# Kernel optimization log

Hardware: AMD Instinct MI355X
Metric: run time of the kernel (lower is better)

## Reference

```python
import jax, jax.numpy as jnp
import numpy as np

NUM_HEADS = 8
SIGMA = 1.0
LAMBDA_INIT = 0.1
GAMMA_INIT = 0.001


def _pos_encoding(H, W, d_model):
    # 2D sinusoidal encoding: first half encodes x (width), second half y (height)
    d = d_model // 2
    div = jnp.exp(jnp.arange(0, d, 2, dtype=jnp.float32) * (-np.log(10000.0) / d))
    xs = jnp.arange(W, dtype=jnp.float32)[:, None] * div  # (W, d//2)
    ys = jnp.arange(H, dtype=jnp.float32)[:, None] * div  # (H, d//2)
    pe_x = jnp.stack([jnp.sin(xs), jnp.cos(xs)], axis=-1).reshape(W, d)
    pe_y = jnp.stack([jnp.sin(ys), jnp.cos(ys)], axis=-1).reshape(H, d)
    pe = jnp.concatenate([
        jnp.broadcast_to(pe_x[None, :, :], (H, W, d)),
        jnp.broadcast_to(pe_y[:, None, :], (H, W, d)),
    ], axis=-1)
    return pe  # (H, W, d_model)


def _distance_map(H, W, sigma):
    # exp(-euclidean_dist / sigma) between all flattened pixel positions
    yy, xx = jnp.meshgrid(jnp.arange(H, dtype=jnp.float32), jnp.arange(W, dtype=jnp.float32), indexing='ij')
    coords = jnp.stack([yy.reshape(-1), xx.reshape(-1)], axis=-1)  # (HW, 2)
    d2 = jnp.sum((coords[:, None, :] - coords[None, :, :]) ** 2, axis=-1)
    return jnp.exp(-jnp.sqrt(d2) / sigma)  # (HW, HW)


def _conv1x1(x, w, b):
    # 1x1 conv == channel matmul; x: (B,C,H,W), w: (O,C), b: (O,)
    return jnp.einsum('bchw,oc->bohw', x, w) + b[None, :, None, None]


def setup_inputs() -> dict:
    key = jax.random.key(0)
    ks = jax.random.split(key, 9)
    B, C, H, W = 2, 256, 48, 48
    d_model = 256
    inp = {
        'x': jax.random.normal(ks[0], (B, C, H, W), dtype=jnp.float32),
        'Wq': jax.random.normal(ks[1], (d_model, C), dtype=jnp.float32) * 0.01,
        'bq': jnp.zeros((d_model,), dtype=jnp.float32),
        'Wk': jax.random.normal(ks[2], (d_model, C), dtype=jnp.float32) * 0.01,
        'bk': jnp.zeros((d_model,), dtype=jnp.float32),
        'Wv': jax.random.normal(ks[3], (d_model, C), dtype=jnp.float32) * 0.01,
        'bv': jnp.zeros((d_model,), dtype=jnp.float32),
        'Wo': jax.random.normal(ks[4], (C, d_model), dtype=jnp.float32) * 0.01,
        'bo': jnp.zeros((C,), dtype=jnp.float32),
        'lambda_dist': jnp.float32(LAMBDA_INIT),
        'gamma': jnp.float32(GAMMA_INIT),
    }
    return inp


def reference(x, Wq, bq, Wk, bk, Wv, bv, Wo, bo, lambda_dist, gamma):
    B, C, H, W = x.shape
    d_model = Wq.shape[0]
    d_k = d_model // NUM_HEADS
    pe = _pos_encoding(H, W, d_model).transpose(2, 0, 1)[None]  # (1, d_model, H, W)
    dm = _distance_map(H, W, SIGMA)                              # (HW, HW)

    q = _conv1x1(x, Wq, bq) + pe
    k = _conv1x1(x, Wk, bk) + pe
    v = _conv1x1(x, Wv, bv)

    def heads(t):
        return t.reshape(B, NUM_HEADS, d_k, H * W).transpose(0, 1, 3, 2)  # (B,h,HW,d_k)

    Q, K, V = heads(q), heads(k), heads(v)
    scores = jnp.einsum('bhnd,bhmd->bhnm', Q, K) / jnp.sqrt(jnp.float32(d_k))
    scores = scores + (lambda_dist * dm)[None, None]  # 'exp' distance prior bias
    attn = jax.nn.softmax(scores, axis=-1)
    out = jnp.einsum('bhnm,bhmd->bhnd', attn, V)
    out = out.transpose(0, 1, 3, 2).reshape(B, d_model, H, W)
    fused = gamma * out  # simple weighted fusion, single (self) branch
    return x + _conv1x1(fused, Wo, bo)
```

## Files before the change

### kernel.cpp

```cpp
#include <hip/hip_runtime.h>

#define HW 2304
#define SW 48
#define DMODEL 256
#define NHEADS 8
#define DK 32
#define BATCH 2

typedef unsigned short u16;
typedef __attribute__((ext_vector_type(8))) short short8;
typedef __attribute__((ext_vector_type(4))) float f32x4;

__device__ __forceinline__ float bf2f(u16 v) {
  union { unsigned int u; float f; } c; c.u = ((unsigned int)v) << 16; return c.f;
}
__device__ __forceinline__ u16 f2bf(float f) {
  union { unsigned int u; float f; } c; c.f = f;
  unsigned int u = c.u;
  unsigned int r = (u + 0x7FFFu + ((u >> 16) & 1u)) >> 16;
  return (u16)r;
}
__device__ __forceinline__ int div48(int n) { return (n * 87382) >> 22; }
__device__ __forceinline__ int swz(int row, int k) {
  return ((row >> 4) << 12) + ((k >> 3) << 7) + ((row & 15) << 3) + (k & 7);
}

#define DTAB_N 9032

__global__ __launch_bounds__(256) void prep_kernel(
    const float* __restrict__ x,
    const float* __restrict__ Wq, const float* __restrict__ Wk,
    const float* __restrict__ Wv, const float* __restrict__ Wo,
    const float* __restrict__ lam_p,
    u16* __restrict__ xt, u16* __restrict__ Wb, u16* __restrict__ dtabb) {
  int bid = blockIdx.x;
  int t = threadIdx.x;
  if (bid < 288) {
    int b = bid / 144, r = bid % 144;
    int c0 = (r / 36) * 64, n0 = (r % 36) * 64;
    __shared__ u16 sh[64][72];
#pragma unroll
    for (int p = 0; p < 4; ++p) {
      int row = (t >> 4) + p * 16;
      int col4 = (t & 15) * 4;
      float4 v = *(const float4*)(x + (size_t)(b * DMODEL + c0 + row) * HW +
                                  n0 + col4);
      sh[col4 + 0][row] = f2bf(v.x);
      sh[col4 + 1][row] = f2bf(v.y);
      sh[col4 + 2][row] = f2bf(v.z);
      sh[col4 + 3][row] = f2bf(v.w);
    }
    __syncthreads();
    u16* xtb = xt + (size_t)b * HW * DMODEL;
#pragma unroll
    for (int q = 0; q < 2; ++q) {
      int nrow = t >> 2;
      int c8 = (t & 3) * 8 + q * 32;
      *(uint4*)(xtb + swz(n0 + nrow, c0 + c8)) = *(const uint4*)&sh[nrow][c8];
    }
  } else if (bid < 544) {
    int idx = (bid - 288) * 1024 + t * 4;
    int which = idx >> 16, off = idx & 65535;
    int m = off >> 8, k = off & 255;
    const float* src = (which == 0) ? Wq : (which == 1) ? Wk
                       : (which == 2) ? Wv : Wo;
    float4 v = *(const float4*)(src + off);
    ushort4 ov;
    ov.x = f2bf(v.x); ov.y = f2bf(v.y); ov.z = f2bf(v.z); ov.w = f2bf(v.w);
    *(ushort4*)(Wb + which * 65536 + swz(m, k)) = ov;
  } else {
    int id = (bid - 544) * 256 + t;
    if (id < DTAB_N) {
      float v = 0.f;
      if (id < 95 * 95) {
        float lam = lam_p[0];
        int dyi = id / 95, dxi = id - dyi * 95;
        float dy = (float)(dyi - 47), dx = (float)(dxi - 47);
        v = lam * expf(-sqrtf(dy * dy + dx * dx));
      }
      dtabb[id] = f2bf(v);
    }
  }
}

__global__ __launch_bounds__(256) void qkv_kernel(
    const u16* __restrict__ Wb, const u16* __restrict__ xt,
    const float* __restrict__ bq, const float* __restrict__ bk,
    const float* __restrict__ bv,
    u16* __restrict__ qt, u16* __restrict__ ktb, u16* __restrict__ vb) {
  int t = threadIdx.x;
  int w = t >> 6, lane = t & 63, lo = lane & 15, quad = lane >> 4;
  int n0 = blockIdx.x * 64;
  int mb = blockIdx.y, b = blockIdx.z;
  int which = mb >> 2;
  int mrel0 = (mb & 3) * 64;
  const u16* A = Wb + which * 65536 + ((mrel0 + w * 16) >> 4) * 4096 + lo * 8;
  const float* bias = (which == 0) ? bq : (which == 1) ? bk : bv;
  const u16* Bx = xt + (size_t)b * HW * DMODEL + lo * 8;

  f32x4 acc[4] = {{0.f, 0.f, 0.f, 0.f}, {0.f, 0.f, 0.f, 0.f},
                  {0.f, 0.f, 0.f, 0.f}, {0.f, 0.f, 0.f, 0.f}};
#pragma unroll
  for (int k0 = 0; k0 < DMODEL; k0 += 32) {
    int kblk = ((k0 >> 3) + quad) << 7;
    short8 af = *(const short8*)(A + kblk);
#pragma unroll
    for (int nt = 0; nt < 4; ++nt) {
      short8 bf_ = *(const short8*)(Bx + ((n0 + nt * 16) >> 4) * 4096 + kblk);
      acc[nt] = __builtin_amdgcn_mfma_f32_16x16x32_bf16(af, bf_, acc[nt], 0, 0, 0);
    }
  }

  int mbase = mrel0 + w * 16 + quad * 4;
  if (which == 2) {
#pragma unroll
    for (int reg = 0; reg < 4; ++reg) {
      int mrel = mbase + reg;
      float bi = bias[mrel];
      u16* dst = vb + (size_t)(b * DMODEL + mrel) * HW + n0 + lo;
#pragma unroll
      for (int nt = 0; nt < 4; ++nt) dst[nt * 16] = f2bf(acc[nt][reg] + bi);
    }
  } else {
    float sc = (which == 0) ? 0.17677669529663687f : 1.0f;
    int h = mbase >> 5, d0 = mbase & 31;
    u16* base = ((which == 0) ? qt : ktb) + (size_t)(b * NHEADS + h) * HW * DK;
    float bi[4], dv[4];
    bool usecos[4], usey[4];
#pragma unroll
    for (int reg = 0; reg < 4; ++reg) {
      int mrel = mbase + reg;
      bi[reg] = bias[mrel];
      int oo = mrel & 127;
      dv[reg] = expf(-0.07195578415606394f * (float)(oo & ~1));
      usecos[reg] = (oo & 1);
      usey[reg] = (mrel >= 128);
    }
#pragma unroll
    for (int nt = 0; nt < 4; ++nt) {
      int n = n0 + nt * 16 + lo;
      int yy = div48(n), xx = n - yy * SW;
      ushort4 ov;
      float vals[4];
#pragma unroll
      for (int reg = 0; reg < 4; ++reg) {
        float tv = (usey[reg] ? (float)yy : (float)xx) * dv[reg];
        float pe = usecos[reg] ? cosf(tv) : sinf(tv);
        vals[reg] = (acc[nt][reg] + bi[reg] + pe) * sc;
      }
      ov.x = f2bf(vals[0]); ov.y = f2bf(vals[1]);
      ov.z = f2bf(vals[2]); ov.w = f2bf(vals[3]);
      *(ushort4*)(base + (size_t)n * DK + d0) = ov;
    }
  }
}

__global__ __launch_bounds__(256) void attn_kernel(
    const u16* __restrict__ qt, const u16* __restrict__ ktb,
    const u16* __restrict__ vb, const u16* __restrict__ dtabb,
    u16* __restrict__ aot) {
  int t = threadIdx.x;
  int w = t >> 6;
  int lane = t & 63;
  int lo = lane & 15, quad = lane >> 4;
  int n0 = blockIdx.x * 64;
  int h = blockIdx.y, b = blockIdx.z;

  __shared__ __align__(16) u16 dsh[DTAB_N];
  __shared__ u16 Ks[64 * 40];
  __shared__ u16 Vs[32 * 72];
  __shared__ u16 Ps[4 * 16 * 72];

  for (int i = t; i < DTAB_N / 8; i += 256)
    *(uint4*)&dsh[i * 8] = *(const uint4*)&dtabb[i * 8];

  const u16* qtg = qt + (size_t)(b * NHEADS + h) * HW * DK;
  const u16* ktg = ktb + (size_t)(b * NHEADS + h) * HW * DK;
  const u16* vbg = vb + (size_t)(b * DMODEL + h * DK) * HW;

  short8 qf = *(const short8*)(qtg + (size_t)(n0 + w * 16 + lo) * DK + quad * 8);

  int a_i[4];
#pragma unroll
  for (int reg = 0; reg < 4; ++reg) {
    int n = n0 + w * 16 + quad * 4 + reg;
    int y1 = div48(n), x1 = n - y1 * SW;
    a_i[reg] = y1 * 95 + x1 + 4512;
  }

  f32x4 o0 = {0.f, 0.f, 0.f, 0.f}, o1 = {0.f, 0.f, 0.f, 0.f};
  float lsum[4] = {0.f, 0.f, 0.f, 0.f};
  u16* psw = Ps + w * 16 * 72;

  for (int kt = 0; kt < 36; ++kt) {
    int m0 = kt * 64;
    __syncthreads();
    {
      int row = t >> 2, c8 = (t & 3) * 8;
      *(uint4*)&Ks[row * 40 + c8] =
          *(const uint4*)(ktg + (size_t)(m0 + row) * DK + c8);
      int dd = t >> 3, mo = (t & 7) * 8;
      *(uint4*)&Vs[dd * 72 + mo] =
          *(const uint4*)(vbg + (size_t)dd * HW + m0 + mo);
    }
    __syncthreads();

    f32x4 s[4];
#pragma unroll
    for (int t4 = 0; t4 < 4; ++t4) {
      short8 kf = *(const short8*)&Ks[(t4 * 16 + lo) * 40 + quad * 8];
      f32x4 z = {0.f, 0.f, 0.f, 0.f};
      s[t4] = __builtin_amdgcn_mfma_f32_16x16x32_bf16(qf, kf, z, 0, 0, 0);
    }
#pragma unroll
    for (int t4 = 0; t4 < 4; ++t4) {
      int m = m0 + t4 * 16 + lo;
      int y2 = div48(m), x2 = m - y2 * SW;
      int bj = y2 * 95 + x2;
#pragma unroll
      for (int reg = 0; reg < 4; ++reg) {
        float p = __expf(s[t4][reg] + bf2f(dsh[a_i[reg] - bj]));
        lsum[reg] += p;
        psw[(quad * 4 + reg) * 72 + t4 * 16 + lo] = f2bf(p);
      }
    }
#pragma unroll
    for (int ks = 0; ks < 2; ++ks) {
      short8 af = *(const short8*)&psw[lo * 72 + ks * 32 + quad * 8];
      short8 v0 = *(const short8*)&Vs[lo * 72 + ks * 32 + quad * 8];
      o0 = __builtin_amdgcn_mfma_f32_16x16x32_bf16(af, v0, o0, 0, 0, 0);
      short8 v1 = *(const short8*)&Vs[(16 + lo) * 72 + ks * 32 + quad * 8];
      o1 = __builtin_amdgcn_mfma_f32_16x16x32_bf16(af, v1, o1, 0, 0, 0);
    }
  }

#pragma unroll
  for (int d = 1; d < 16; d <<= 1) {
#pragma unroll
    for (int reg = 0; reg < 4; ++reg) lsum[reg] += __shfl_xor(lsum[reg], d);
  }

  u16* aog = aot + (size_t)b * HW * DMODEL;
#pragma unroll
  for (int reg = 0; reg < 4; ++reg) {
    int n = n0 + w * 16 + quad * 4 + reg;
    float inv = 1.0f / lsum[reg];
    aog[swz(n, h * DK + lo)] = f2bf(o0[reg] * inv);
    aog[swz(n, h * DK + 16 + lo)] = f2bf(o1[reg] * inv);
  }
}

__global__ __launch_bounds__(256) void out_kernel(
    const float* __restrict__ x, const u16* __restrict__ Wob,
    const float* __restrict__ bo, const float* __restrict__ gp,
    const u16* __restrict__ aot, float* __restrict__ out) {
  int t = threadIdx.x;
  int w = t >> 6, lane = t & 63, lo = lane & 15, quad = lane >> 4;
  int n0 = blockIdx.x * 64;
  int c0 = blockIdx.y * 64;
  int b = blockIdx.z;
  float gamma = gp[0];
  const u16* A = Wob + ((c0 + w * 16) >> 4) * 4096 + lo * 8;
  const u16* Ba = aot + (size_t)b * HW * DMODEL + lo * 8;

  f32x4 acc[4] = {{0.f, 0.f, 0.f, 0.f}, {0.f, 0.f, 0.f, 0.f},
                  {0.f, 0.f, 0.f, 0.f}, {0.f, 0.f, 0.f, 0.f}};
#pragma unroll
  for (int k0 = 0; k0 < DMODEL; k0 += 32) {
    int kblk = ((k0 >> 3) + quad) << 7;
    short8 af = *(const short8*)(A + kblk);
#pragma unroll
    for (int nt = 0; nt < 4; ++nt) {
      short8 bf_ = *(const short8*)(Ba + ((n0 + nt * 16) >> 4) * 4096 + kblk);
      acc[nt] = __builtin_amdgcn_mfma_f32_16x16x32_bf16(af, bf_, acc[nt], 0, 0, 0);
    }
  }

#pragma unroll
  for (int reg = 0; reg < 4; ++reg) {
    int c = c0 + w * 16 + quad * 4 + reg;
    float bi = bo[c];
    const float* xs = x + (size_t)(b * DMODEL + c) * HW + n0 + lo;
    float* os = out + (size_t)(b * DMODEL + c) * HW + n0 + lo;
#pragma unroll
    for (int nt = 0; nt < 4; ++nt)
      os[nt * 16] = xs[nt * 16] + gamma * acc[nt][reg] + bi;
  }
}

extern "C" void kernel_launch(void* const* d_in, const int* in_sizes, int n_in,
                              void* d_out, int out_size, void* d_ws,
                              size_t ws_size, hipStream_t stream) {
  const float* x   = (const float*)d_in[0];
  const float* Wq  = (const float*)d_in[1];
  const float* bq  = (const float*)d_in[2];
  const float* Wk  = (const float*)d_in[3];
  const float* bk  = (const float*)d_in[4];
  const float* Wv  = (const float*)d_in[5];
  const float* bv  = (const float*)d_in[6];
  const float* Wo  = (const float*)d_in[7];
  const float* bo  = (const float*)d_in[8];
  const float* lam = (const float*)d_in[9];
  const float* gam = (const float*)d_in[10];

  char* wsb = (char*)d_ws;
  u16* dtabb = (u16*)wsb;
  u16* Wb  = (u16*)(wsb + 36864);
  u16* xt  = (u16*)(wsb + 561152);
  u16* aot = xt;
  u16* qt  = (u16*)(wsb + 2920448);
  u16* ktb = (u16*)(wsb + 5279744);
  u16* vb  = (u16*)(wsb + 7639040);
  float* out = (float*)d_out;

  prep_kernel<<<dim3(580), 256, 0, stream>>>(x, Wq, Wk, Wv, Wo, lam,
                                             xt, Wb, dtabb);
  qkv_kernel<<<dim3(36, 12, BATCH), 256, 0, stream>>>(Wb, xt, bq, bk, bv,
                                                      qt, ktb, vb);
  attn_kernel<<<dim3(36, NHEADS, BATCH), 256, 0, stream>>>(qt, ktb, vb, dtabb,
                                                           aot);
  out_kernel<<<dim3(36, 4, BATCH), 256, 0, stream>>>(x, Wb + 3 * 65536, bo, gam,
                                                     aot, out);
}
```

Baseline: 152.0 us.

## Precompute full distance-bias matrix in MFMA tile layout instead of LDS table lookup

Replaces the compact 95x95 distance table, which attn_kernel copied into shared memory and indexed with per-element gathers, with a full HW x HW bf16 bias matrix. A new kernel writes this matrix in a tile order that matches the MFMA output layout, so each lane reads its four bias values with one 8-byte global load per tile. This removes the LDS table fill, the div48 index arithmetic and the scattered LDS reads from the softmax loop, and lowers LDS use. In exchange it adds about 10 MB of bias traffic, which each of the 16 (batch, head) blocks reads again from L2 or HBM, plus an extra kernel launch.

```diff
diff --git a/kernel.cpp b/kernel.cpp
--- a/kernel.cpp
+++ b/kernel.cpp
@@ -14,6 +14,12 @@
 __device__ __forceinline__ float bf2f(u16 v) {
   union { unsigned int u; float f; } c; c.u = ((unsigned int)v) << 16; return c.f;
 }
+__device__ __forceinline__ float lo2f(unsigned int u) {
+  union { unsigned int u; float f; } c; c.u = u << 16; return c.f;
+}
+__device__ __forceinline__ float hi2f(unsigned int u) {
+  union { unsigned int u; float f; } c; c.u = u & 0xffff0000u; return c.f;
+}
 __device__ __forceinline__ u16 f2bf(float f) {
   union { unsigned int u; float f; } c; c.f = f;
   unsigned int u = c.u;
@@ -25,14 +31,34 @@
   return ((row >> 4) << 12) + ((k >> 3) << 7) + ((row & 15) << 3) + (k & 7);
 }
 
-#define DTAB_N 9032
+__global__ __launch_bounds__(256) void eb_kernel(const float* __restrict__ lam_p,
+                                                 u16* __restrict__ et) {
+  int id = blockIdx.x * 256 + threadIdx.x;
+  int flat = id * 8;
+  int tile = flat >> 8;
+  int within = flat & 255;
+  int tm = tile / 144, tq = tile - tm * 144;
+  int m = tm * 16 + (within >> 4);
+  int q = tq * 16 + (within & 15);
+  int ym = div48(m), xm = m - ym * SW;
+  int yq = div48(q), xq = q - yq * SW;
+  float lam = lam_p[0];
+  float dy = (float)(yq - ym);
+  float dy2 = dy * dy;
+  u16 o[8];
+#pragma unroll
+  for (int j = 0; j < 8; ++j) {
+    float dx = (float)(xq + j - xm);
+    o[j] = f2bf(lam * __expf(-sqrtf(dy2 + dx * dx)));
+  }
+  *(uint4*)(et + flat) = *(const uint4*)o;
+}
 
 __global__ __launch_bounds__(256) void prep_kernel(
     const float* __restrict__ x,
     const float* __restrict__ Wq, const float* __restrict__ Wk,
     const float* __restrict__ Wv, const float* __restrict__ Wo,
-    const float* __restrict__ lam_p,
-    u16* __restrict__ xt, u16* __restrict__ Wb, u16* __restrict__ dtabb) {
+    u16* __restrict__ xt, u16* __restrict__ Wb) {
   int bid = blockIdx.x;
   int t = threadIdx.x;
   if (bid < 288) {
@@ -58,7 +84,7 @@
       int c8 = (t & 3) * 8 + q * 32;
       *(uint4*)(xtb + swz(n0 + nrow, c0 + c8)) = *(const uint4*)&sh[nrow][c8];
     }
-  } else if (bid < 544) {
+  } else {
     int idx = (bid - 288) * 1024 + t * 4;
     int which = idx >> 16, off = idx & 65535;
     int m = off >> 8, k = off & 255;
@@ -68,18 +94,6 @@
     ushort4 ov;
     ov.x = f2bf(v.x); ov.y = f2bf(v.y); ov.z = f2bf(v.z); ov.w = f2bf(v.w);
     *(ushort4*)(Wb + which * 65536 + swz(m, k)) = ov;
-  } else {
-    int id = (bid - 544) * 256 + t;
-    if (id < DTAB_N) {
-      float v = 0.f;
-      if (id < 95 * 95) {
-        float lam = lam_p[0];
-        int dyi = id / 95, dxi = id - dyi * 95;
-        float dy = (float)(dyi - 47), dx = (float)(dxi - 47);
-        v = lam * expf(-sqrtf(dy * dy + dx * dx));
-      }
-      dtabb[id] = f2bf(v);
-    }
   }
 }
 
@@ -157,7 +171,7 @@
 
 __global__ __launch_bounds__(256) void attn_kernel(
     const u16* __restrict__ qt, const u16* __restrict__ ktb,
-    const u16* __restrict__ vb, const u16* __restrict__ dtabb,
+    const u16* __restrict__ vb, const u16* __restrict__ et,
     u16* __restrict__ aot) {
   int t = threadIdx.x;
   int w = t >> 6;
@@ -166,27 +180,18 @@
   int n0 = blockIdx.x * 64;
   int h = blockIdx.y, b = blockIdx.z;
 
-  __shared__ __align__(16) u16 dsh[DTAB_N];
   __shared__ u16 Ks[64 * 40];
   __shared__ u16 Vs[32 * 72];
   __shared__ u16 Ps[4 * 16 * 72];
 
-  for (int i = t; i < DTAB_N / 8; i += 256)
-    *(uint4*)&dsh[i * 8] = *(const uint4*)&dtabb[i * 8];
-
   const u16* qtg = qt + (size_t)(b * NHEADS + h) * HW * DK;
   const u16* ktg = ktb + (size_t)(b * NHEADS + h) * HW * DK;
   const u16* vbg = vb + (size_t)(b * DMODEL + h * DK) * HW;
 
   short8 qf = *(const short8*)(qtg + (size_t)(n0 + w * 16 + lo) * DK + quad * 8);
 
-  int a_i[4];
-#pragma unroll
-  for (int reg = 0; reg < 4; ++reg) {
-    int n = n0 + w * 16 + quad * 4 + reg;
-    int y1 = div48(n), x1 = n - y1 * SW;
-    a_i[reg] = y1 * 95 + x1 + 4512;
-  }
+  int tq = (n0 >> 4) + w;
+  const u16* etw = et + (size_t)tq * 256 + lo * 16 + quad * 4;
 
   f32x4 o0 = {0.f, 0.f, 0.f, 0.f}, o1 = {0.f, 0.f, 0.f, 0.f};
   float lsum[4] = {0.f, 0.f, 0.f, 0.f};
@@ -205,6 +210,11 @@
     }
     __syncthreads();
 
+    uint2 ebv[4];
+#pragma unroll
+    for (int t4 = 0; t4 < 4; ++t4)
+      ebv[t4] = *(const uint2*)(etw + (size_t)((m0 >> 4) + t4) * 36864);
+
     f32x4 s[4];
 #pragma unroll
     for (int t4 = 0; t4 < 4; ++t4) {
@@ -214,15 +224,15 @@
     }
 #pragma unroll
     for (int t4 = 0; t4 < 4; ++t4) {
-      int m = m0 + t4 * 16 + lo;
-      int y2 = div48(m), x2 = m - y2 * SW;
-      int bj = y2 * 95 + x2;
-#pragma unroll
-      for (int reg = 0; reg < 4; ++reg) {
-        float p = __expf(s[t4][reg] + bf2f(dsh[a_i[reg] - bj]));
-        lsum[reg] += p;
-        psw[(quad * 4 + reg) * 72 + t4 * 16 + lo] = f2bf(p);
-      }
+      float p0 = __expf(s[t4][0] + lo2f(ebv[t4].x));
+      float p1 = __expf(s[t4][1] + hi2f(ebv[t4].x));
+      float p2 = __expf(s[t4][2] + lo2f(ebv[t4].y));
+      float p3 = __expf(s[t4][3] + hi2f(ebv[t4].y));
+      lsum[0] += p0; lsum[1] += p1; lsum[2] += p2; lsum[3] += p3;
+      psw[(quad * 4 + 0) * 72 + t4 * 16 + lo] = f2bf(p0);
+      psw[(quad * 4 + 1) * 72 + t4 * 16 + lo] = f2bf(p1);
+      psw[(quad * 4 + 2) * 72 + t4 * 16 + lo] = f2bf(p2);
+      psw[(quad * 4 + 3) * 72 + t4 * 16 + lo] = f2bf(p3);
     }
 #pragma unroll
     for (int ks = 0; ks < 2; ++ks) {
@@ -304,20 +314,20 @@
   const float* gam = (const float*)d_in[10];
 
   char* wsb = (char*)d_ws;
-  u16* dtabb = (u16*)wsb;
   u16* Wb  = (u16*)(wsb + 36864);
   u16* xt  = (u16*)(wsb + 561152);
   u16* aot = xt;
   u16* qt  = (u16*)(wsb + 2920448);
   u16* ktb = (u16*)(wsb + 5279744);
   u16* vb  = (u16*)(wsb + 7639040);
+  u16* et  = (u16*)(wsb + 9998336);
   float* out = (float*)d_out;
 
-  prep_kernel<<<dim3(580), 256, 0, stream>>>(x, Wq, Wk, Wv, Wo, lam,
-                                             xt, Wb, dtabb);
+  eb_kernel<<<dim3(2592), 256, 0, stream>>>(lam, et);
+  prep_kernel<<<dim3(544), 256, 0, stream>>>(x, Wq, Wk, Wv, Wo, xt, Wb);
   qkv_kernel<<<dim3(36, 12, BATCH), 256, 0, stream>>>(Wb, xt, bq, bk, bv,
                                                       qt, ktb, vb);
-  attn_kernel<<<dim3(36, NHEADS, BATCH), 256, 0, stream>>>(qt, ktb, vb, dtabb,
+  attn_kernel<<<dim3(36, NHEADS, BATCH), 256, 0, stream>>>(qt, ktb, vb, et,
                                                            aot);
   out_kernel<<<dim3(36, 4, BATCH), 256, 0, stream>>>(x, Wb + 3 * 65536, bo, gam,
                                                      aot, out);
```

Measured after the change: 151.3 us. About the same (-0.5%).
